# Performance work log

Measured on AMD Instinct MI355X. Metric: run time of the kernel, lower is better.

Reference implementation:

```python
import jax, jax.numpy as jnp
import numpy as np

CONF_THR = 0.3   # cfg.THRESHOLD_PREDICT_CONF
NMS_THR = 0.5    # cfg.THRESHOLD_PREDICT_NMS
TOPK = 500       # hard-coded topk(500) in forward


def _build_grid():
    # YOLOv3 @416: scales 13/26/52, 3 anchors each -> 10647 rows
    sizes = [13, 26, 52]
    anc = np.array([[10, 13], [16, 30], [33, 23], [30, 61], [62, 45], [59, 119],
                    [116, 90], [156, 198], [373, 326]], np.float32) / 416.0
    groups = [anc[6:9], anc[3:6], anc[0:3]]  # large anchors on coarse grid
    grids, anchors, fs = [], [], []
    for s, g in zip(sizes, groups):
        ys, xs = np.meshgrid(np.arange(s), np.arange(s), indexing='ij')
        gxy = np.stack([xs, ys], -1).astype(np.float32)          # [s,s,2]
        gxy = np.repeat(gxy.reshape(-1, 1, 2), 3, axis=1).reshape(-1, 2)
        grids.append(gxy)
        anchors.append(np.tile(g[None], (s * s, 1, 1)).reshape(-1, 2))
        fs.append(np.full((s * s * 3, 1), float(s), np.float32))
    return (np.concatenate(grids).astype(np.float32),
            np.concatenate(anchors).astype(np.float32),
            np.concatenate(fs).astype(np.float32))


def setup_inputs() -> dict:
    key = jax.random.key(0)
    k1, k2, k3 = jax.random.split(key, 3)
    B, A, C = 64, 10647, 80
    g, aw, fs = _build_grid()
    return {
        "pconf": jax.random.normal(k1, (B, A, 1), jnp.float32),
        "pcls": jax.random.normal(k2, (B, A, C), jnp.float32),
        "ptxywh": jax.random.normal(k3, (B, A, 4), jnp.float32),
        "grid_xy": jnp.asarray(g),
        "anchor_wh": jnp.asarray(aw),
        "fsize": jnp.asarray(fs),
    }


def _decode(ptxywh, grid_xy, anchor_wh, fsize):
    # boxes_decode4yolo3: sigmoid xy offset + cell, exp wh * anchor (all normalized)
    xy = (jax.nn.sigmoid(ptxywh[..., :2]) + grid_xy) / fsize   # [B,A,2]
    wh = jnp.exp(ptxywh[..., 2:]) * anchor_wh                  # [B,A,2]
    return jnp.concatenate([xy - 0.5 * wh, xy + 0.5 * wh], -1)  # ltrb


def _pairwise_iou(b):  # b: [K,4] ltrb
    area = jnp.maximum(b[:, 2] - b[:, 0], 0.) * jnp.maximum(b[:, 3] - b[:, 1], 0.)
    lt = jnp.maximum(b[:, None, :2], b[None, :, :2])
    rb = jnp.minimum(b[:, None, 2:], b[None, :, 2:])
    wh = jnp.maximum(rb - lt, 0.)
    inter = wh[..., 0] * wh[..., 1]
    return inter / (area[:, None] + area[None, :] - inter + 1e-9)


def _label_nms(boxes, labels, valid, thr):
    # boxes are pre-sorted by descending score (lax.top_k output order)
    K = boxes.shape[0]
    sup = (_pairwise_iou(boxes) > thr) & (labels[:, None] == labels[None, :])
    idx = jnp.arange(K)

    def body(suppressed, i):
        keep_i = valid[i] & ~suppressed[i]
        suppressed = suppressed | (keep_i & sup[i] & (idx > i))
        return suppressed, keep_i

    _, keep = jax.lax.scan(body, jnp.zeros(K, bool), idx)
    return keep


def reference(pconf, pcls, ptxywh, grid_xy, anchor_wh, fsize):
    B, A, _ = ptxywh.shape
    conf = jax.nn.sigmoid(pconf)[..., 0]            # [B,A]
    pc = jax.nn.sigmoid(pcls)                       # [B,A,C]
    cls_conf = pc.max(-1)
    plabels = pc.argmax(-1)
    pscores = cls_conf * conf                       # [B,A]

    vals, idx = jax.lax.top_k(pscores, TOPK)        # sorted desc, [B,K]
    valid = vals > CONF_THR                         # mask_pos AND mask_topk

    pltrb = _decode(ptxywh, grid_xy, anchor_wh, fsize)          # [B,A,4]
    boxes = jnp.take_along_axis(pltrb, idx[..., None], axis=1)  # [B,K,4]
    boxes = jnp.clip(boxes, 0.0, 1.0)
    labels = jnp.take_along_axis(plabels, idx, axis=1) + 1      # 1-based

    keep = jax.vmap(_label_nms, in_axes=(0, 0, 0, None))(boxes, labels, valid, NMS_THR)
    ids_batch = jnp.broadcast_to(jnp.arange(B)[:, None], (B, TOPK))
    return ids_batch, boxes, labels, vals, keep
```

## Files before the change

### kernel.cpp

```cpp
#include <hip/hip_runtime.h>
#include <math.h>

#define A_N 10647
#define C_N 80
#define K_N 500
#define CONF_THRF 0.3f
#define NMS_THRF 0.5f

#define NBUCK 1024
#define CAND_N 2048

#define SC_BLOCKS 2048

typedef float f32x4 __attribute__((ext_vector_type(4)));

__device__ __forceinline__ float sigmoid_ref(float x) {
    float e = expf(-x);
    return 1.0f / (1.0f + e);
}

__device__ __forceinline__ unsigned long long shfl_u64(unsigned long long v, int src) {
    unsigned int lo = (unsigned int)v, hi = (unsigned int)(v >> 32);
    lo = __shfl(lo, src, 64);
    hi = __shfl(hi, src, 64);
    return ((unsigned long long)hi << 32) | (unsigned long long)lo;
}

__device__ __forceinline__ unsigned long long shfl_xor_u64(unsigned long long v, int mask) {
    unsigned int lo = (unsigned int)v, hi = (unsigned int)(v >> 32);
    lo = __shfl_xor(lo, mask, 64);
    hi = __shfl_xor(hi, mask, 64);
    return ((unsigned long long)hi << 32) | (unsigned long long)lo;
}

__device__ __forceinline__ void reduce_row(
    const f32x4 v[5], int sub, float pc, size_t row,
    float* __restrict__ scores, int* __restrict__ labels) {
    float m = -3.4e38f;
    #pragma unroll
    for (int j = 0; j < 5; ++j)
        m = fmaxf(m, fmaxf(fmaxf(v[j][0], v[j][1]), fmaxf(v[j][2], v[j][3])));
    m = fmaxf(m, __shfl_xor(m, 1, 64));
    m = fmaxf(m, __shfl_xor(m, 2, 64));

    const float win = m - 1e-4f;
    int imin = 0x7FFFFFFF, cnt = 0;
    #pragma unroll
    for (int j = 0; j < 5; ++j) {
        #pragma unroll
        for (int t = 0; t < 4; ++t) {
            int idx = (sub + 4 * j) * 4 + t;
            if (v[j][t] == m && idx < imin) imin = idx;
            cnt += (v[j][t] >= win) ? 1 : 0;
        }
    }
    {
        int o = __shfl_xor(imin, 1, 64); imin = imin < o ? imin : o;
        o = __shfl_xor(imin, 2, 64);     imin = imin < o ? imin : o;
        cnt += __shfl_xor(cnt, 1, 64);
        cnt += __shfl_xor(cnt, 2, 64);
    }

    float sbest; int ibest;
    if (cnt >= 2) {
        unsigned long long key = 0ull;
        #pragma unroll
        for (int j = 0; j < 5; ++j) {
            #pragma unroll
            for (int t = 0; t < 4; ++t) {
                float x = v[j][t];
                if (x >= win) {
                    int idx = (sub + 4 * j) * 4 + t;
                    float s = sigmoid_ref(x);
                    unsigned long long k =
                        ((unsigned long long)__float_as_uint(s) << 32) |
                        (unsigned long long)(0xFFFFu - (unsigned)idx);
                    if (k > key) key = k;
                }
            }
        }
        unsigned long long o = shfl_xor_u64(key, 1); if (o > key) key = o;
        o = shfl_xor_u64(key, 2);                    if (o > key) key = o;
        sbest = __uint_as_float((unsigned int)(key >> 32));
        ibest = 0xFFFF - (int)(key & 0xFFFFull);
    } else {
        sbest = sigmoid_ref(m);
        ibest = imin;
    }

    if (sub == 0) {
        float cf = sigmoid_ref(pc);
        __builtin_nontemporal_store(__fmul_rn(sbest, cf), scores + row);
        __builtin_nontemporal_store(ibest, labels + row);
    }
}

__global__ __launch_bounds__(256) void score_kernel(
    const float* __restrict__ pconf,
    const float* __restrict__ pcls,
    float* __restrict__ scores,
    int* __restrict__ labels,
    int nrows) {
    const int tid = threadIdx.x;
    const int sub = tid & 3;
    int row = (blockIdx.x * 256 + tid) >> 2;
    const int stride = (SC_BLOCKS * 256) >> 2;
    if (row >= nrows) return;

    f32x4 v[5];
    {
        const f32x4* rp = (const f32x4*)(pcls + (size_t)row * C_N);
        #pragma unroll
        for (int j = 0; j < 5; ++j) v[j] = __builtin_nontemporal_load(rp + sub + 4 * j);
    }
    float pc = __builtin_nontemporal_load(pconf + row);

    while (true) {
        const int rown = row + stride;
        const bool hasn = rown < nrows;
        f32x4 v2[5];
        float pcn = 0.0f;
        if (hasn) {
            const f32x4* rp = (const f32x4*)(pcls + (size_t)rown * C_N);
            #pragma unroll
            for (int j = 0; j < 5; ++j) v2[j] = __builtin_nontemporal_load(rp + sub + 4 * j);
            pcn = __builtin_nontemporal_load(pconf + rown);
        }

        reduce_row(v, sub, pc, (size_t)row, scores, labels);

        if (!hasn) break;
        #pragma unroll
        for (int j = 0; j < 5; ++j) v[j] = v2[j];
        pc = pcn;
        row = rown;
    }
}

__global__ __launch_bounds__(1024) void topk_nms_kernel(
    const float* __restrict__ scores,
    const int* __restrict__ labels,
    const float* __restrict__ ptxywh,
    const float* __restrict__ grid_xy,
    const float* __restrict__ anchor_wh,
    const float* __restrict__ fsize,
    float* __restrict__ out, int B) {
    extern __shared__ unsigned char smem[];
    unsigned int* hist = (unsigned int*)smem;
    unsigned long long* cand = (unsigned long long*)(smem + 4096);
    unsigned int* cntp = (unsigned int*)(smem + 20480);
    unsigned int* Tp   = (unsigned int*)(smem + 20484);
    const int b = blockIdx.x;
    const int tid = threadIdx.x;
    const float* sb = scores + (size_t)b * A_N;

    hist[tid] = 0u;
    cand[tid] = 0ull;
    cand[tid + 1024] = 0ull;
    if (tid == 0) *cntp = 0u;
    __syncthreads();

    for (int i = tid; i < A_N; i += 1024) {
        unsigned int u = __float_as_uint(sb[i]) >> 20;
        atomicAdd(&hist[u], 1u);
    }
    __syncthreads();

    for (int d = 1; d < NBUCK; d <<= 1) {
        unsigned int v = (tid + d < NBUCK) ? hist[tid + d] : 0u;
        __syncthreads();
        hist[tid] += v;
        __syncthreads();
    }
    if (hist[tid] >= K_N && (tid == NBUCK - 1 || hist[tid + 1] < K_N)) *Tp = (unsigned)tid;
    __syncthreads();
    const unsigned int T = *Tp;
    __syncthreads();

    for (int i = tid; i < A_N; i += 1024) {
        unsigned int u = __float_as_uint(sb[i]);
        if ((u >> 20) >= T) {
            unsigned int slot = atomicAdd(cntp, 1u);
            if (slot < CAND_N)
                cand[slot] = ((unsigned long long)u << 32) |
                             (unsigned long long)(0xFFFFu - (unsigned)i);
        }
    }
    __syncthreads();

    for (int sz = 2; sz <= CAND_N; sz <<= 1) {
        for (int j = sz >> 1; j > 0; j >>= 1) {
            int i = ((tid & ~(j - 1)) << 1) | (tid & (j - 1));
            int l = i | j;
            unsigned long long a = cand[i];
            unsigned long long c = cand[l];
            bool descBlk = ((i & sz) == 0);
            if (descBlk ? (a < c) : (a > c)) { cand[i] = c; cand[l] = a; }
            __syncthreads();
        }
    }

    unsigned long long myk = 0ull;
    if (tid < K_N) myk = cand[tid];
    __syncthreads();

    float* bxL   = (float*)smem;
    float* areaL = (float*)(smem + 8000);
    int*   labL  = (int*)  (smem + 10000);
    float* valsL = (float*)(smem + 12000);
    unsigned long long* nzL   = (unsigned long long*)(smem + 14016);
    unsigned long long* keepL = (unsigned long long*)(smem + 14080);
    unsigned long long* supL  = (unsigned long long*)(smem + 14336);

    if (tid >= 512 && tid < 520) nzL[tid - 512] = 0ull;

    const size_t BK = (size_t)B * K_N;
    if (tid < K_N) {
        float scv = __uint_as_float((unsigned int)(myk >> 32));
        int idx = 0xFFFF - (int)(myk & 0xFFFFull);
        int lb = labels[(size_t)b * A_N + idx] + 1;
        const float* t4 = ptxywh + ((size_t)b * A_N + idx) * 4;
        float tx = t4[0], ty = t4[1], tw = t4[2], th = t4[3];
        float gx = grid_xy[idx * 2 + 0], gy = grid_xy[idx * 2 + 1];
        float aw = anchor_wh[idx * 2 + 0], ah = anchor_wh[idx * 2 + 1];
        float fs = fsize[idx];
        float cx = __fdiv_rn(__fadd_rn(sigmoid_ref(tx), gx), fs);
        float cy = __fdiv_rn(__fadd_rn(sigmoid_ref(ty), gy), fs);
        float wx = __fmul_rn(expf(tw), aw);
        float wy = __fmul_rn(expf(th), ah);
        float hx = __fmul_rn(0.5f, wx);
        float hy = __fmul_rn(0.5f, wy);
        float x0 = __fsub_rn(cx, hx), y0 = __fsub_rn(cy, hy);
        float x1 = __fadd_rn(cx, hx), y1 = __fadd_rn(cy, hy);
        x0 = fminf(fmaxf(x0, 0.0f), 1.0f);
        y0 = fminf(fmaxf(y0, 0.0f), 1.0f);
        x1 = fminf(fmaxf(x1, 0.0f), 1.0f);
        y1 = fminf(fmaxf(y1, 0.0f), 1.0f);
        float area = __fmul_rn(fmaxf(__fsub_rn(x1, x0), 0.0f),
                               fmaxf(__fsub_rn(y1, y0), 0.0f));
        bxL[tid * 4 + 0] = x0; bxL[tid * 4 + 1] = y0;
        bxL[tid * 4 + 2] = x1; bxL[tid * 4 + 3] = y1;
        areaL[tid] = area; labL[tid] = lb; valsL[tid] = scv;

        out[(size_t)b * K_N + tid] = (float)b;
        float* ob = out + BK + ((size_t)b * K_N + tid) * 4;
        ob[0] = x0; ob[1] = y0; ob[2] = x1; ob[3] = y1;
        out[5 * BK + (size_t)b * K_N + tid] = (float)lb;
        out[6 * BK + (size_t)b * K_N + tid] = scv;
    }
    __syncthreads();

    for (int task = tid; task < K_N * 8; task += 1024) {
        int i = task >> 3;
        int w = task & 7;
        float li = bxL[i * 4 + 0], ti = bxL[i * 4 + 1];
        float ri = bxL[i * 4 + 2], bi = bxL[i * 4 + 3];
        float ai = areaL[i];
        int lbi = labL[i];
        unsigned long long bits = 0ull;
        int j0 = w * 64;
        int jend = j0 + 64; if (jend > K_N) jend = K_N;
        int jst = j0 > i + 1 ? j0 : i + 1;
        for (int j = jst; j < jend; ++j) {
            if (labL[j] == lbi) {
                float lj = bxL[j * 4 + 0], tj = bxL[j * 4 + 1];
                float rj = bxL[j * 4 + 2], bj = bxL[j * 4 + 3];
                float ltx = fmaxf(li, lj), lty = fmaxf(ti, tj);
                float rbx = fminf(ri, rj), rby = fminf(bi, bj);
                float iw = fmaxf(__fsub_rn(rbx, ltx), 0.0f);
                float ih = fmaxf(__fsub_rn(rby, lty), 0.0f);
                float inter = __fmul_rn(iw, ih);
                float den = __fadd_rn(__fsub_rn(__fadd_rn(ai, areaL[j]), inter), 1e-9f);
                float iou = __fdiv_rn(inter, den);
                if (iou > NMS_THRF) bits |= (1ull << (j - j0));
            }
        }
        supL[i * 8 + w] = bits;
        if (bits) atomicOr(&nzL[i >> 6], 1ull << (i & 63));
    }
    __syncthreads();

    if (tid < 64) {
        const int lane = tid;
        unsigned long long supp = 0ull, keepm = 0ull;
        unsigned long long nzreg = (lane < 8) ? nzL[lane] : 0ull;
        #pragma unroll
        for (int t = 0; t < 8; ++t) {
            const int i0 = t * 64;
            int myi = i0 + lane;
            bool v = (myi < K_N) ? (valsL[myi] > CONF_THRF) : false;
            unsigned long long vword = __ballot(v);
            unsigned long long nzword = shfl_u64(nzreg, t);
            const int imax = (K_N - i0 < 64) ? (K_N - i0) : 64;
            for (int i2 = 0; i2 < imax; ++i2) {
                unsigned long long sw = shfl_u64(supp, t);
                bool keep_i = ((vword >> i2) & 1ull) && !((sw >> i2) & 1ull);
                if (keep_i) {
                    if (lane == t) keepm |= (1ull << i2);
                    if ((nzword >> i2) & 1ull) {
                        if (lane < 8) supp |= supL[(i0 + i2) * 8 + lane];
                    }
                }
            }
        }
        if (lane < 8) keepL[lane] = keepm;
    }
    __syncthreads();

    if (tid < K_N) {
        unsigned long long kw = keepL[tid >> 6];
        out[7 * BK + (size_t)b * K_N + tid] = (float)((kw >> (tid & 63)) & 1ull);
    }
}

extern "C" void kernel_launch(void* const* d_in, const int* in_sizes, int n_in,
                              void* d_out, int out_size, void* d_ws, size_t ws_size,
                              hipStream_t stream) {
    const float* pconf     = (const float*)d_in[0];
    const float* pcls      = (const float*)d_in[1];
    const float* ptxywh    = (const float*)d_in[2];
    const float* grid_xy   = (const float*)d_in[3];
    const float* anchor_wh = (const float*)d_in[4];
    const float* fsize     = (const float*)d_in[5];
    int total = in_sizes[0];
    int B = total / A_N;
    if (B <= 0) return;

    float* scores = (float*)d_ws;
    int*   labls  = (int*)((char*)d_ws + (size_t)total * sizeof(float));
    float* out    = (float*)d_out;

    hipLaunchKernelGGL(score_kernel, dim3(SC_BLOCKS), dim3(256), 0, stream,
                       pconf, pcls, scores, labls, total);
    hipLaunchKernelGGL(topk_nms_kernel, dim3(B), dim3(1024), 46592, stream,
                       scores, labls, ptxywh, grid_xy, anchor_wh, fsize, out, B);
}
```

Before: 158.4 us.

## Skip class reduction for rows whose confidence bound cannot reach top-K

```diff
diff --git a/kernel.cpp b/kernel.cpp
--- a/kernel.cpp
+++ b/kernel.cpp
@@ -9,14 +9,18 @@
 
 #define NBUCK 1024
 #define CAND_N 2048
-
-#define SC_BLOCKS 2048
+#define CAND_TARGET 600
 
 typedef float f32x4 __attribute__((ext_vector_type(4)));
 
 __device__ __forceinline__ float sigmoid_ref(float x) {
     float e = expf(-x);
     return 1.0f / (1.0f + e);
+}
+
+__device__ __forceinline__ unsigned bucket_of(float v) {
+    unsigned u = __float_as_uint(v) >> 20;
+    return u > 1023u ? 1023u : u;
 }
 
 __device__ __forceinline__ unsigned long long shfl_u64(unsigned long long v, int src) {
@@ -33,9 +37,8 @@
     return ((unsigned long long)hi << 32) | (unsigned long long)lo;
 }
 
-__device__ __forceinline__ void reduce_row(
-    const f32x4 v[5], int sub, float pc, size_t row,
-    float* __restrict__ scores, int* __restrict__ labels) {
+__device__ __forceinline__ void reduce_core(
+    const f32x4 v[5], int sub, float& sbest, int& ibest) {
     float m = -3.4e38f;
     #pragma unroll
     for (int j = 0; j < 5; ++j)
@@ -61,7 +64,6 @@
         cnt += __shfl_xor(cnt, 2, 64);
     }
 
-    float sbest; int ibest;
     if (cnt >= 2) {
         unsigned long long key = 0ull;
         #pragma unroll
@@ -87,53 +89,110 @@
         sbest = sigmoid_ref(m);
         ibest = imin;
     }
-
-    if (sub == 0) {
-        float cf = sigmoid_ref(pc);
-        __builtin_nontemporal_store(__fmul_rn(sbest, cf), scores + row);
-        __builtin_nontemporal_store(ibest, labels + row);
-    }
-}
-
-__global__ __launch_bounds__(256) void score_kernel(
+}
+
+__global__ __launch_bounds__(1024) void ustar_kernel(
+    const float* __restrict__ pconf,
+    unsigned* __restrict__ ustar,
+    unsigned* __restrict__ shist) {
+    __shared__ unsigned hist[NBUCK];
+    const int b = blockIdx.x, tid = threadIdx.x;
+    hist[tid] = 0u;
+    shist[(size_t)b * NBUCK + tid] = 0u;
+    __syncthreads();
+    for (int i = tid; i < A_N; i += 1024) {
+        float ubv = sigmoid_ref(pconf[(size_t)b * A_N + i]);
+        atomicAdd(&hist[bucket_of(ubv)], 1u);
+    }
+    __syncthreads();
+    for (int d = 1; d < NBUCK; d <<= 1) {
+        unsigned v = (tid + d < NBUCK) ? hist[tid + d] : 0u;
+        __syncthreads();
+        hist[tid] += v;
+        __syncthreads();
+    }
+    if (hist[tid] >= CAND_TARGET && (tid == NBUCK - 1 || hist[tid + 1] < CAND_TARGET))
+        ustar[b] = (unsigned)tid;
+}
+
+__global__ __launch_bounds__(256) void cand_kernel(
     const float* __restrict__ pconf,
     const float* __restrict__ pcls,
     float* __restrict__ scores,
     int* __restrict__ labels,
-    int nrows) {
-    const int tid = threadIdx.x;
-    const int sub = tid & 3;
-    int row = (blockIdx.x * 256 + tid) >> 2;
-    const int stride = (SC_BLOCKS * 256) >> 2;
-    if (row >= nrows) return;
-
-    f32x4 v[5];
-    {
-        const f32x4* rp = (const f32x4*)(pcls + (size_t)row * C_N);
-        #pragma unroll
-        for (int j = 0; j < 5; ++j) v[j] = __builtin_nontemporal_load(rp + sub + 4 * j);
-    }
-    float pc = __builtin_nontemporal_load(pconf + row);
-
-    while (true) {
-        const int rown = row + stride;
-        const bool hasn = rown < nrows;
-        f32x4 v2[5];
-        float pcn = 0.0f;
-        if (hasn) {
-            const f32x4* rp = (const f32x4*)(pcls + (size_t)rown * C_N);
+    const unsigned* __restrict__ ustar,
+    unsigned* __restrict__ shist,
+    int total) {
+    const int sub = threadIdx.x & 3;
+    const int g0 = (blockIdx.x * 256 + threadIdx.x) >> 2;
+    const int gstride = (2048 * 256) >> 2;
+    for (int r = g0; r < total; r += gstride) {
+        unsigned b = (unsigned)r / A_N;
+        float ub = sigmoid_ref(pconf[r]);
+        if (bucket_of(ub) >= ustar[b]) {
+            const f32x4* rp = (const f32x4*)(pcls + (size_t)r * C_N);
+            f32x4 v[5];
             #pragma unroll
-            for (int j = 0; j < 5; ++j) v2[j] = __builtin_nontemporal_load(rp + sub + 4 * j);
-            pcn = __builtin_nontemporal_load(pconf + rown);
-        }
-
-        reduce_row(v, sub, pc, (size_t)row, scores, labels);
-
-        if (!hasn) break;
-        #pragma unroll
-        for (int j = 0; j < 5; ++j) v[j] = v2[j];
-        pc = pcn;
-        row = rown;
+            for (int j = 0; j < 5; ++j) v[j] = rp[sub + 4 * j];
+            float s; int ib;
+            reduce_core(v, sub, s, ib);
+            float sc = __fmul_rn(s, ub);
+            if (sub == 0) {
+                scores[r] = sc;
+                labels[r] = ib;
+                atomicAdd(&shist[(size_t)b * NBUCK + bucket_of(sc)], 1u);
+            }
+        }
+    }
+}
+
+__global__ __launch_bounds__(1024) void tval_kernel(
+    const unsigned* __restrict__ shist,
+    float* __restrict__ tval) {
+    __shared__ unsigned hist[NBUCK];
+    const int b = blockIdx.x, tid = threadIdx.x;
+    hist[tid] = shist[(size_t)b * NBUCK + tid];
+    __syncthreads();
+    for (int d = 1; d < NBUCK; d <<= 1) {
+        unsigned v = (tid + d < NBUCK) ? hist[tid + d] : 0u;
+        __syncthreads();
+        hist[tid] += v;
+        __syncthreads();
+    }
+    if (hist[tid] >= K_N && (tid == NBUCK - 1 || hist[tid + 1] < K_N))
+        tval[b] = __uint_as_float(((unsigned)tid) << 20);
+}
+
+__global__ __launch_bounds__(256) void rest_kernel(
+    const float* __restrict__ pconf,
+    const float* __restrict__ pcls,
+    float* __restrict__ scores,
+    int* __restrict__ labels,
+    const unsigned* __restrict__ ustar,
+    const float* __restrict__ tval,
+    int total) {
+    const int sub = threadIdx.x & 3;
+    const int g0 = (blockIdx.x * 256 + threadIdx.x) >> 2;
+    const int gstride = (2048 * 256) >> 2;
+    for (int r = g0; r < total; r += gstride) {
+        unsigned b = (unsigned)r / A_N;
+        float ub = sigmoid_ref(pconf[r]);
+        unsigned u = bucket_of(ub);
+        if (u >= ustar[b]) continue;
+        if (ub >= tval[b]) {
+            const f32x4* rp = (const f32x4*)(pcls + (size_t)r * C_N);
+            f32x4 v[5];
+            #pragma unroll
+            for (int j = 0; j < 5; ++j) v[j] = rp[sub + 4 * j];
+            float s; int ib;
+            reduce_core(v, sub, s, ib);
+            if (sub == 0) {
+                scores[r] = __fmul_rn(s, ub);
+                labels[r] = ib;
+            }
+        } else if (sub == 0) {
+            scores[r] = 0.0f;
+        }
     }
 }
 
@@ -326,12 +385,21 @@
     int B = total / A_N;
     if (B <= 0) return;
 
-    float* scores = (float*)d_ws;
-    int*   labls  = (int*)((char*)d_ws + (size_t)total * sizeof(float));
-    float* out    = (float*)d_out;
-
-    hipLaunchKernelGGL(score_kernel, dim3(SC_BLOCKS), dim3(256), 0, stream,
-                       pconf, pcls, scores, labls, total);
+    float*    scores = (float*)d_ws;
+    int*      labls  = (int*)((char*)d_ws + (size_t)total * 4);
+    unsigned* shist  = (unsigned*)((char*)d_ws + (size_t)total * 8);
+    unsigned* ustar  = shist + (size_t)B * NBUCK;
+    float*    tval   = (float*)(ustar + B);
+    float*    out    = (float*)d_out;
+
+    hipLaunchKernelGGL(ustar_kernel, dim3(B), dim3(1024), 0, stream,
+                       pconf, ustar, shist);
+    hipLaunchKernelGGL(cand_kernel, dim3(2048), dim3(256), 0, stream,
+                       pconf, pcls, scores, labls, ustar, shist, total);
+    hipLaunchKernelGGL(tval_kernel, dim3(B), dim3(1024), 0, stream,
+                       shist, tval);
+    hipLaunchKernelGGL(rest_kernel, dim3(2048), dim3(256), 0, stream,
+                       pconf, pcls, scores, labls, ustar, tval, total);
     hipLaunchKernelGGL(topk_nms_kernel, dim3(B), dim3(1024), 46592, stream,
                        scores, labls, ptxywh, grid_xy, anchor_wh, fsize, out, B);
 }
```

Result: slower. 177.9 us (+12.4%).
